# Kernel optimization log

Measured on AMD Instinct MI355X. Metric: run time of the kernel, lower is better.

## Reference

```python
import jax, jax.numpy as jnp
import numpy as np

N, IN_DIM, OUT_DIM, HEADS, SUB = 4096, 256, 128, 4, 32
ETA = 0.5
LAMBDA_SPARSE = 0.05
NEG_BIG = -1e9


def setup_inputs() -> dict:
    key = jax.random.key(0)
    k1, k2, k3, k4 = jax.random.split(key, 4)
    H = jax.random.normal(k1, (N, IN_DIM), dtype=jnp.float32)
    # sparse binary adjacency mask (avg degree ~ 41) with self-loops
    adj_mask = (jax.random.uniform(k2, (N, N)) < 0.01).astype(jnp.float32)
    adj_mask = adj_mask.at[jnp.arange(N), jnp.arange(N)].set(1.0)
    # per-head orthonormal subspace bases U_k = QR(randn)[:, :SUB]
    raw = jax.random.normal(k3, (HEADS, IN_DIM, SUB), dtype=jnp.float32)
    U = jax.vmap(lambda r: jnp.linalg.qr(r)[0])(raw)  # [h, D, s]
    threshold = jnp.full((OUT_DIM,), LAMBDA_SPARSE, dtype=jnp.float32)
    proj_w = jax.random.normal(k4, (OUT_DIM, IN_DIM), dtype=jnp.float32) / np.float32(np.sqrt(IN_DIM))
    return {"H": H, "adj_mask": adj_mask, "U": U, "threshold": threshold, "proj_w": proj_w}


def reference(H, adj_mask, U, threshold, proj_w):
    # Z_k = U_k^T @ H^T  -> [h, s, N]
    Z = jnp.einsum('hds,nd->hsn', U, H)
    # scores_k = Z_k^T @ Z_k / sqrt(s)  -> [h, N, N]
    scores = jnp.einsum('hsn,hsm->hnm', Z, Z) / jnp.sqrt(jnp.float32(SUB))
    scores = scores + (1.0 - adj_mask)[None, :, :] * NEG_BIG
    alpha = jax.nn.softmax(scores, axis=-1)  # torch softmax(dim=1) on [N,N] rows
    # agg_k = Z_k @ alpha_k^T  -> [h, s, N];  sum_k U_k @ agg_k -> [D, N]
    agg = jnp.einsum('hsj,hij->hsi', Z, alpha)
    agg_sum = jnp.einsum('hds,hsn->dn', U, agg)
    H_half = H + ETA * agg_sum.T           # [N, D]
    H_half = H_half @ proj_w.T             # [N, out_dim]
    # soft-threshold
    H_out = jnp.sign(H_half) * jax.nn.relu(jnp.abs(H_half) - threshold[None, :])
    # orthogonality loss: sum_k ||U_k^T U_k - I||_F^2 + sum_{k<l} ||U_k^T U_l||_F^2
    G = jnp.einsum('kds,ldt->klst', U, U)  # [h, h, s, s]
    eye_s = jnp.eye(SUB, dtype=U.dtype)
    eye_h = jnp.eye(HEADS, dtype=U.dtype)
    sub = G - eye_h[:, :, None, None] * eye_s[None, None, :, :]
    sq = jnp.sum(sub ** 2, axis=(2, 3))    # [h, h]
    orth_loss = jnp.sum(jnp.triu(jnp.ones((HEADS, HEADS), dtype=U.dtype)) * sq)
    return H_out, orth_loss
```

## Files before the change

### kernel.cpp

```cpp
#include <hip/hip_runtime.h>
#include <hip/hip_bf16.h>
#include <math.h>

#define NN 4096
#define IN_DIM 256
#define OUT_DIM 128
#define HEADS 4
#define SUB 32
#define MAXDEG 128
#define ETA 0.5f
#define INV_SQRT_SUB 0.17677669529663687f

typedef __attribute__((ext_vector_type(8))) short bf16x8;
typedef __attribute__((ext_vector_type(4))) short s16x4;
typedef __attribute__((ext_vector_type(4))) float f32x4;

static __device__ inline short f2bf(float f) {
    unsigned u = __float_as_uint(f);
    unsigned r = u + 0x7FFFu + ((u >> 16) & 1u);
    return (short)(r >> 16);
}
static __device__ inline float bf2f(short s) {
    return __uint_as_float(((unsigned)(unsigned short)s) << 16);
}
#define MFMA16(a, b, c) __builtin_amdgcn_mfma_f32_16x16x32_bf16(a, b, c, 0, 0, 0)

__global__ __launch_bounds__(256) void fused_small(const float* __restrict__ U,
                                                   const float* __restrict__ PW,
                                                   short* __restrict__ Wh,
                                                   short* __restrict__ Wl,
                                                   float* __restrict__ W2,
                                                   float* __restrict__ loss_parts) {
    int b = blockIdx.x;
    int t = threadIdx.x;
    __shared__ float sh[260];

    if (b < 256) {
        float v;
        if (b < 128) {
            int h = b >> 5, s = b & 31;
            v = U[h * IN_DIM * SUB + t * SUB + s];
        } else {
            v = PW[(b - 128) * IN_DIM + t];
        }
        short hi = f2bf(v);
        Wh[b * IN_DIM + t] = hi;
        Wl[b * IN_DIM + t] = f2bf(v - bf2f(hi));
    } else if (b < 384) {
        int hs = b - 256;
        int h = hs >> 5, s = hs & 31;
        sh[t] = U[h * IN_DIM * SUB + t * SUB + s];
        __syncthreads();
        if (t < 128) {
            const float4* pw4 = (const float4*)(PW + t * IN_DIM);
            const float4* u4  = (const float4*)sh;
            float acc = 0.f;
            #pragma unroll 4
            for (int d4 = 0; d4 < 64; ++d4) {
                float4 a = u4[d4], p = pw4[d4];
                acc += a.x * p.x + a.y * p.y + a.z * p.z + a.w * p.w;
            }
            W2[hs * OUT_DIM + t] = acc;
        }
    } else {
        const int pk[10] = {0,0,0,0,1,1,1,2,2,3};
        const int pl[10] = {0,1,2,3,1,2,3,2,3,3};
        int p = b - 384;
        int k = pk[p], l = pl[p];
        int t2 = t & 31;
        int sg = t >> 5;
        const float* Uk = U + k * IN_DIM * SUB;
        const float* Ul = U + l * IN_DIM * SUB;
        float a0 = 0.f, a1 = 0.f, a2 = 0.f, a3 = 0.f;
        #pragma unroll 4
        for (int d = 0; d < IN_DIM; ++d) {
            float ul = Ul[d * SUB + t2];
            float u0 = Uk[d * SUB + sg * 4 + 0];
            float u1 = Uk[d * SUB + sg * 4 + 1];
            float u2 = Uk[d * SUB + sg * 4 + 2];
            float u3 = Uk[d * SUB + sg * 4 + 3];
            a0 += u0 * ul; a1 += u1 * ul; a2 += u2 * ul; a3 += u3 * ul;
        }
        if (k == l) {
            if (sg * 4 + 0 == t2) a0 -= 1.f;
            if (sg * 4 + 1 == t2) a1 -= 1.f;
            if (sg * 4 + 2 == t2) a2 -= 1.f;
            if (sg * 4 + 3 == t2) a3 -= 1.f;
        }
        float local = a0 * a0 + a1 * a1 + a2 * a2 + a3 * a3;
        local += __shfl_xor(local, 32, 64);
        local += __shfl_xor(local, 16, 64);
        local += __shfl_xor(local, 8, 64);
        local += __shfl_xor(local, 4, 64);
        local += __shfl_xor(local, 2, 64);
        local += __shfl_xor(local, 1, 64);
        if ((t & 63) == 0) sh[256 + (t >> 6)] = local;
        __syncthreads();
        if (t == 0) loss_parts[p] = sh[256] + sh[257] + sh[258] + sh[259];
    }
}

#define LDA 264
__global__ __launch_bounds__(256) void ztp_mfma(const float* __restrict__ H,
                                                const short* __restrict__ Wh,
                                                const short* __restrict__ Wl,
                                                float* __restrict__ ZT,
                                                float* __restrict__ P) {
    __shared__ short Ah[16 * LDA];
    __shared__ short Al[16 * LDA];
    int t = threadIdx.x, b = blockIdx.x;
    int m0 = (b >> 1) * 16, chalf = b & 1;

    {
        int r = t >> 4, dbase = (t & 15) * 16;
        const float4* src = (const float4*)(H + (size_t)(m0 + r) * IN_DIM + dbase);
        #pragma unroll
        for (int q = 0; q < 4; ++q) {
            float4 f = src[q];
            float fv[4] = {f.x, f.y, f.z, f.w};
            s16x4 hi, lo;
            #pragma unroll
            for (int j = 0; j < 4; ++j) {
                short h = f2bf(fv[j]);
                hi[j] = h;
                lo[j] = f2bf(fv[j] - bf2f(h));
            }
            *(s16x4*)&Ah[r * LDA + dbase + q * 4] = hi;
            *(s16x4*)&Al[r * LDA + dbase + q * 4] = lo;
        }
    }
    __syncthreads();

    int wave = t >> 6, lane = t & 63;
    int c0 = chalf * 128 + wave * 32;
    int arow = lane & 15, agrp = lane >> 4;

    const short* ahp = &Ah[arow * LDA + agrp * 8];
    const short* alp = &Al[arow * LDA + agrp * 8];
    const short* bh0 = Wh + (size_t)(c0 + arow) * IN_DIM + agrp * 8;
    const short* bl0 = Wl + (size_t)(c0 + arow) * IN_DIM + agrp * 8;
    const short* bh1 = bh0 + 16 * IN_DIM;
    const short* bl1 = bl0 + 16 * IN_DIM;

    f32x4 acc0 = {0.f, 0.f, 0.f, 0.f};
    f32x4 acc1 = {0.f, 0.f, 0.f, 0.f};

    #pragma unroll
    for (int kk = 0; kk < 8; ++kk) {
        int d0 = kk * 32;
        bf16x8 a_h = *(const bf16x8*)(ahp + d0);
        bf16x8 a_l = *(const bf16x8*)(alp + d0);
        bf16x8 b0h = *(const bf16x8*)(bh0 + d0);
        bf16x8 b0l = *(const bf16x8*)(bl0 + d0);
        bf16x8 b1h = *(const bf16x8*)(bh1 + d0);
        bf16x8 b1l = *(const bf16x8*)(bl1 + d0);
        acc0 = MFMA16(a_h, b0h, acc0);
        acc0 = MFMA16(a_h, b0l, acc0);
        acc0 = MFMA16(a_l, b0h, acc0);
        acc1 = MFMA16(a_h, b1h, acc1);
        acc1 = MFMA16(a_h, b1l, acc1);
        acc1 = MFMA16(a_l, b1h, acc1);
    }

    float* dst = chalf ? P : ZT;
    int colbase = c0 - chalf * 128;
    #pragma unroll
    for (int i = 0; i < 4; ++i) {
        int row = m0 + agrp * 4 + i;
        dst[(size_t)row * 128 + colbase + arow]      = acc0[i];
        dst[(size_t)row * 128 + colbase + 16 + arow] = acc1[i];
    }
}

__global__ __launch_bounds__(128) void attn_core(const float* __restrict__ ZT,
                                                 const float* __restrict__ adj,
                                                 float* __restrict__ agg) {
    int i = blockIdx.x;
    int t = threadIdx.x;
    __shared__ int   nbr_s[MAXDEG];
    __shared__ float e_s[MAXDEG][HEADS];
    __shared__ float z_s[128];
    __shared__ int cnt;

    const float4* row4 = (const float4*)(adj + (size_t)i * NN);
    float4 v[8];
    #pragma unroll
    for (int k = 0; k < 8; ++k) v[k] = row4[t + k * 128];

    if (t == 0) cnt = 0;
    nbr_s[t] = 0;
    z_s[t] = ZT[(size_t)i * 128 + t];
    __syncthreads();

    #pragma unroll
    for (int k = 0; k < 8; ++k) {
        int j0 = (t + k * 128) * 4;
        if (v[k].x > 0.5f) { int p = atomicAdd(&cnt, 1); if (p < MAXDEG) nbr_s[p] = j0; }
        if (v[k].y > 0.5f) { int p = atomicAdd(&cnt, 1); if (p < MAXDEG) nbr_s[p] = j0 + 1; }
        if (v[k].z > 0.5f) { int p = atomicAdd(&cnt, 1); if (p < MAXDEG) nbr_s[p] = j0 + 2; }
        if (v[k].w > 0.5f) { int p = atomicAdd(&cnt, 1); if (p < MAXDEG) nbr_s[p] = j0 + 3; }
    }
    __syncthreads();
    int dg = cnt < MAXDEG ? cnt : MAXDEG;

    int jj0 = t >> 2, h = t & 3;
    int ntiles = (dg + 31) >> 5;
    const float4* qr = (const float4*)(&z_s[h * 32]);
    for (int tile = 0; tile < ntiles; ++tile) {
        int jj = tile * 32 + jj0;
        int j = nbr_s[jj];
        const float4* zr = (const float4*)(ZT + (size_t)j * 128 + h * 32);
        float acc = 0.f;
        #pragma unroll
        for (int k = 0; k < 8; ++k) {
            float4 z = zr[k];
            float4 q = qr[k];
            acc += z.x * q.x + z.y * q.y + z.z * q.z + z.w * q.w;
        }
        e_s[jj][h] = (jj < dg) ? __expf(acc * INV_SQRT_SUB) : 0.f;
    }
    __syncthreads();

    int hh = t >> 5;
    float accV = 0.f, accS = 0.f;
    const float* zbase = ZT + t;
    for (int jj = 0; jj < dg; jj += 4) {
        int ja = nbr_s[jj],     jb = nbr_s[jj + 1];
        int jc = nbr_s[jj + 2], jd = nbr_s[jj + 3];
        float ea = e_s[jj][hh],     eb = e_s[jj + 1][hh];
        float ec = e_s[jj + 2][hh], ed = e_s[jj + 3][hh];
        float va = zbase[(size_t)ja * 128], vb = zbase[(size_t)jb * 128];
        float vc = zbase[(size_t)jc * 128], vd = zbase[(size_t)jd * 128];
        accV += ea * va + eb * vb + ec * vc + ed * vd;
        accS += (ea + eb) + (ec + ed);
    }
    agg[(size_t)i * 128 + t] = accV * (ETA / accS);
}

#define EROWS 16
__global__ __launch_bounds__(256) void epilogue(const float* __restrict__ Pm,
                                                const float* __restrict__ agg,
                                                const float* __restrict__ W2,
                                                const float* __restrict__ threshold,
                                                const float* __restrict__ loss_parts,
                                                float* __restrict__ out) {
    int t = threadIdx.x;
    int o = t & 127, half = t >> 7;
    int r0 = blockIdx.x * EROWS;
    __shared__ float As[EROWS][128];
    const float4* a4 = (const float4*)(agg + (size_t)r0 * 128);
    float4* As4 = (float4*)&As[0][0];
    As4[t]       = a4[t];
    As4[t + 256] = a4[t + 256];

    if (blockIdx.x == 0 && t == 0) {
        float L = 0.f;
        #pragma unroll
        for (int p = 0; p < 10; ++p) L += loss_parts[p];
        out[(size_t)NN * OUT_DIM] = L;
    }
    __syncthreads();

    float acc[8];
    #pragma unroll
    for (int r = 0; r < 8; ++r) acc[r] = 0.f;

    for (int q4 = 0; q4 < 32; ++q4) {
        int hs = q4 * 4;
        float w0 = W2[(hs + 0) * 128 + o];
        float w1 = W2[(hs + 1) * 128 + o];
        float w2v = W2[(hs + 2) * 128 + o];
        float w3 = W2[(hs + 3) * 128 + o];
        #pragma unroll
        for (int r = 0; r < 8; ++r) {
            float4 a = *(const float4*)&As[half * 8 + r][hs];
            acc[r] += a.x * w0 + a.y * w1 + a.z * w2v + a.w * w3;
        }
    }
    float th = threshold[o];
    #pragma unroll
    for (int r = 0; r < 8; ++r) {
        int row = r0 + half * 8 + r;
        float val = Pm[(size_t)row * 128 + o] + acc[r];
        float av = fabsf(val) - th;
        out[(size_t)row * 128 + o] = (av > 0.f) ? copysignf(av, val) : 0.f;
    }
}

extern "C" void kernel_launch(void* const* d_in, const int* in_sizes, int n_in,
                              void* d_out, int out_size, void* d_ws, size_t ws_size,
                              hipStream_t stream) {
    const float* H   = (const float*)d_in[0];
    const float* adj = (const float*)d_in[1];
    const float* U   = (const float*)d_in[2];
    const float* thr = (const float*)d_in[3];
    const float* PW  = (const float*)d_in[4];
    float* out = (float*)d_out;

    char* ws = (char*)d_ws;
    float* ZT    = (float*)(ws);
    float* P     = (float*)(ws + (size_t)2097152);
    float* agg   = (float*)(ws + (size_t)4194304);
    float* W2    = (float*)(ws + (size_t)6291456);
    short* Wh    = (short*)(ws + (size_t)6356992);
    short* Wl    = (short*)(ws + (size_t)6488064);
    float* lossp = (float*)(ws + (size_t)6619136);

    fused_small<<<394, 256, 0, stream>>>(U, PW, Wh, Wl, W2, lossp);
    ztp_mfma<<<NN / 16 * 2, 256, 0, stream>>>(H, Wh, Wl, ZT, P);
    attn_core<<<NN, 128, 0, stream>>>(ZT, adj, agg);
    epilogue<<<NN / EROWS, 256, 0, stream>>>(P, agg, W2, thr, lossp, out);
}
```

Baseline: 151.7 us.

## Fuse attention aggregation with epilogue projection and soft-threshold into one kernel

```diff
diff --git a/kernel.cpp b/kernel.cpp
--- a/kernel.cpp
+++ b/kernel.cpp
@@ -29,7 +29,7 @@
                                                    const float* __restrict__ PW,
                                                    short* __restrict__ Wh,
                                                    short* __restrict__ Wl,
-                                                   float* __restrict__ W2,
+                                                   float* __restrict__ W2T,
                                                    float* __restrict__ loss_parts) {
     int b = blockIdx.x;
     int t = threadIdx.x;
@@ -60,7 +60,7 @@
                 float4 a = u4[d4], p = pw4[d4];
                 acc += a.x * p.x + a.y * p.y + a.z * p.z + a.w * p.w;
             }
-            W2[hs * OUT_DIM + t] = acc;
+            W2T[t * OUT_DIM + hs] = acc;
         }
     } else {
         const int pk[10] = {0,0,0,0,1,1,1,2,2,3};
@@ -172,43 +172,56 @@
     }
 }
 
-__global__ __launch_bounds__(128) void attn_core(const float* __restrict__ ZT,
-                                                 const float* __restrict__ adj,
-                                                 float* __restrict__ agg) {
-    int i = blockIdx.x;
-    int t = threadIdx.x;
-    __shared__ int   nbr_s[MAXDEG];
-    __shared__ float e_s[MAXDEG][HEADS];
-    __shared__ float z_s[128];
-    __shared__ int cnt;
-
-    const float4* row4 = (const float4*)(adj + (size_t)i * NN);
+__global__ __launch_bounds__(256) void attn_fused(const float* __restrict__ ZT,
+                                                  const float* __restrict__ Pm,
+                                                  const float* __restrict__ W2T,
+                                                  const float* __restrict__ adj,
+                                                  const float* __restrict__ threshold,
+                                                  const float* __restrict__ loss_parts,
+                                                  float* __restrict__ out) {
+    int b = blockIdx.x, t = threadIdx.x;
+    int half = t >> 7, u = t & 127;
+    int row = b * 2 + half;
+    __shared__ int   nbr_s[2][MAXDEG];
+    __shared__ float e_s[2][MAXDEG][HEADS];
+    __shared__ float z_s[2][128];
+    __shared__ float agg_s[2][128];
+    __shared__ int cnt[2];
+
+    if (b == 0 && t == 0) {
+        float L = 0.f;
+        #pragma unroll
+        for (int p = 0; p < 10; ++p) L += loss_parts[p];
+        out[(size_t)NN * OUT_DIM] = L;
+    }
+
+    const float4* row4 = (const float4*)(adj + (size_t)row * NN);
     float4 v[8];
     #pragma unroll
-    for (int k = 0; k < 8; ++k) v[k] = row4[t + k * 128];
-
-    if (t == 0) cnt = 0;
-    nbr_s[t] = 0;
-    z_s[t] = ZT[(size_t)i * 128 + t];
+    for (int k = 0; k < 8; ++k) v[k] = row4[u + k * 128];
+
+    if (u == 0) cnt[half] = 0;
+    nbr_s[half][u] = 0;
+    z_s[half][u] = ZT[(size_t)row * 128 + u];
     __syncthreads();
 
     #pragma unroll
     for (int k = 0; k < 8; ++k) {
-        int j0 = (t + k * 128) * 4;
-        if (v[k].x > 0.5f) { int p = atomicAdd(&cnt, 1); if (p < MAXDEG) nbr_s[p] = j0; }
-        if (v[k].y > 0.5f) { int p = atomicAdd(&cnt, 1); if (p < MAXDEG) nbr_s[p] = j0 + 1; }
-        if (v[k].z > 0.5f) { int p = atomicAdd(&cnt, 1); if (p < MAXDEG) nbr_s[p] = j0 + 2; }
-        if (v[k].w > 0.5f) { int p = atomicAdd(&cnt, 1); if (p < MAXDEG) nbr_s[p] = j0 + 3; }
-    }
-    __syncthreads();
-    int dg = cnt < MAXDEG ? cnt : MAXDEG;
-
-    int jj0 = t >> 2, h = t & 3;
+        int j0 = (u + k * 128) * 4;
+        if (v[k].x > 0.5f) { int p = atomicAdd(&cnt[half], 1); if (p < MAXDEG) nbr_s[half][p] = j0; }
+        if (v[k].y > 0.5f) { int p = atomicAdd(&cnt[half], 1); if (p < MAXDEG) nbr_s[half][p] = j0 + 1; }
+        if (v[k].z > 0.5f) { int p = atomicAdd(&cnt[half], 1); if (p < MAXDEG) nbr_s[half][p] = j0 + 2; }
+        if (v[k].w > 0.5f) { int p = atomicAdd(&cnt[half], 1); if (p < MAXDEG) nbr_s[half][p] = j0 + 3; }
+    }
+    __syncthreads();
+    int dg = cnt[half] < MAXDEG ? cnt[half] : MAXDEG;
+
+    int jj0 = u >> 2, h = u & 3;
     int ntiles = (dg + 31) >> 5;
-    const float4* qr = (const float4*)(&z_s[h * 32]);
+    const float4* qr = (const float4*)(&z_s[half][h * 32]);
     for (int tile = 0; tile < ntiles; ++tile) {
         int jj = tile * 32 + jj0;
-        int j = nbr_s[jj];
+        int j = nbr_s[half][jj];
         const float4* zr = (const float4*)(ZT + (size_t)j * 128 + h * 32);
         float acc = 0.f;
         #pragma unroll
@@ -217,74 +230,37 @@
             float4 q = qr[k];
             acc += z.x * q.x + z.y * q.y + z.z * q.z + z.w * q.w;
         }
-        e_s[jj][h] = (jj < dg) ? __expf(acc * INV_SQRT_SUB) : 0.f;
-    }
-    __syncthreads();
-
-    int hh = t >> 5;
+        e_s[half][jj][h] = (jj < dg) ? __expf(acc * INV_SQRT_SUB) : 0.f;
+    }
+    __syncthreads();
+
+    int hh = u >> 5;
     float accV = 0.f, accS = 0.f;
-    const float* zbase = ZT + t;
+    const float* zbase = ZT + u;
     for (int jj = 0; jj < dg; jj += 4) {
-        int ja = nbr_s[jj],     jb = nbr_s[jj + 1];
-        int jc = nbr_s[jj + 2], jd = nbr_s[jj + 3];
-        float ea = e_s[jj][hh],     eb = e_s[jj + 1][hh];
-        float ec = e_s[jj + 2][hh], ed = e_s[jj + 3][hh];
+        int ja = nbr_s[half][jj],     jb = nbr_s[half][jj + 1];
+        int jc = nbr_s[half][jj + 2], jd = nbr_s[half][jj + 3];
+        float ea = e_s[half][jj][hh],     eb = e_s[half][jj + 1][hh];
+        float ec = e_s[half][jj + 2][hh], ed = e_s[half][jj + 3][hh];
         float va = zbase[(size_t)ja * 128], vb = zbase[(size_t)jb * 128];
         float vc = zbase[(size_t)jc * 128], vd = zbase[(size_t)jd * 128];
         accV += ea * va + eb * vb + ec * vc + ed * vd;
         accS += (ea + eb) + (ec + ed);
     }
-    agg[(size_t)i * 128 + t] = accV * (ETA / accS);
-}
-
-#define EROWS 16
-__global__ __launch_bounds__(256) void epilogue(const float* __restrict__ Pm,
-                                                const float* __restrict__ agg,
-                                                const float* __restrict__ W2,
-                                                const float* __restrict__ threshold,
-                                                const float* __restrict__ loss_parts,
-                                                float* __restrict__ out) {
-    int t = threadIdx.x;
-    int o = t & 127, half = t >> 7;
-    int r0 = blockIdx.x * EROWS;
-    __shared__ float As[EROWS][128];
-    const float4* a4 = (const float4*)(agg + (size_t)r0 * 128);
-    float4* As4 = (float4*)&As[0][0];
-    As4[t]       = a4[t];
-    As4[t + 256] = a4[t + 256];
-
-    if (blockIdx.x == 0 && t == 0) {
-        float L = 0.f;
-        #pragma unroll
-        for (int p = 0; p < 10; ++p) L += loss_parts[p];
-        out[(size_t)NN * OUT_DIM] = L;
-    }
-    __syncthreads();
-
-    float acc[8];
-    #pragma unroll
-    for (int r = 0; r < 8; ++r) acc[r] = 0.f;
-
-    for (int q4 = 0; q4 < 32; ++q4) {
-        int hs = q4 * 4;
-        float w0 = W2[(hs + 0) * 128 + o];
-        float w1 = W2[(hs + 1) * 128 + o];
-        float w2v = W2[(hs + 2) * 128 + o];
-        float w3 = W2[(hs + 3) * 128 + o];
-        #pragma unroll
-        for (int r = 0; r < 8; ++r) {
-            float4 a = *(const float4*)&As[half * 8 + r][hs];
-            acc[r] += a.x * w0 + a.y * w1 + a.z * w2v + a.w * w3;
-        }
-    }
-    float th = threshold[o];
-    #pragma unroll
-    for (int r = 0; r < 8; ++r) {
-        int row = r0 + half * 8 + r;
-        float val = Pm[(size_t)row * 128 + o] + acc[r];
-        float av = fabsf(val) - th;
-        out[(size_t)row * 128 + o] = (av > 0.f) ? copysignf(av, val) : 0.f;
-    }
+    agg_s[half][u] = accV * (ETA / accS);
+    __syncthreads();
+
+    float val = Pm[(size_t)row * 128 + u];
+    const float4* w4 = (const float4*)(W2T + u * 128);
+    const float4* a4 = (const float4*)(&agg_s[half][0]);
+    #pragma unroll 8
+    for (int k = 0; k < 32; ++k) {
+        float4 w = w4[k], a = a4[k];
+        val += w.x * a.x + w.y * a.y + w.z * a.z + w.w * a.w;
+    }
+    float th = threshold[u];
+    float av = fabsf(val) - th;
+    out[(size_t)row * 128 + u] = (av > 0.f) ? copysignf(av, val) : 0.f;
 }
 
 extern "C" void kernel_launch(void* const* d_in, const int* in_sizes, int n_in,
@@ -300,14 +276,12 @@
     char* ws = (char*)d_ws;
     float* ZT    = (float*)(ws);
     float* P     = (float*)(ws + (size_t)2097152);
-    float* agg   = (float*)(ws + (size_t)4194304);
-    float* W2    = (float*)(ws + (size_t)6291456);
-    short* Wh    = (short*)(ws + (size_t)6356992);
-    short* Wl    = (short*)(ws + (size_t)6488064);
-    float* lossp = (float*)(ws + (size_t)6619136);
-
-    fused_small<<<394, 256, 0, stream>>>(U, PW, Wh, Wl, W2, lossp);
+    float* W2T   = (float*)(ws + (size_t)4194304);
+    short* Wh    = (short*)(ws + (size_t)4259840);
+    short* Wl    = (short*)(ws + (size_t)4390912);
+    float* lossp = (float*)(ws + (size_t)4521984);
+
+    fused_small<<<394, 256, 0, stream>>>(U, PW, Wh, Wl, W2T, lossp);
     ztp_mfma<<<NN / 16 * 2, 256, 0, stream>>>(H, Wh, Wl, ZT, P);
-    attn_core<<<NN, 128, 0, stream>>>(ZT, adj, agg);
-    epilogue<<<NN / EROWS, 256, 0, stream>>>(P, agg, W2, thr, lossp, out);
-}
+    attn_fused<<<NN / 2, 256, 0, stream>>>(ZT, P, W2T, adj, thr, lossp, out);
+}
```

New measurement: 172.0 us. 1.13x slower.
